# Kernel optimization log

Measured on AMD Instinct MI355X. Metric: run time of the kernel, lower is better.

## Reference

```python
import jax, jax.numpy as jnp
import numpy as np

B, R, SR, K, F = 1, 4096, 40, 8, 32
H = 256           # shading_feature_num
NVF = 4           # num_viewdir_freqs -> 2*4*3 = 24 PE channels
EPS = 1e-8


def positional_encoding(x, n_freqs):
    # x: [..., 3] -> [..., 2*n_freqs*3]
    freqs = (2.0 ** jnp.arange(n_freqs)).astype(x.dtype)          # [nf]
    ang = x[..., None, :] * freqs[:, None]                        # [..., nf, 3]
    enc = jnp.concatenate([jnp.sin(ang), jnp.cos(ang)], axis=-1)  # [..., nf, 6]
    return enc.reshape(x.shape[:-1] + (2 * n_freqs * 3,))


def setup_inputs() -> dict:
    key = jax.random.key(0)
    ks = jax.random.split(key, 20)
    s = 0.02
    inp = {
        "sampled_embedding": jax.random.normal(ks[0], (B, R, SR, K, F), jnp.float32),
        "dists": jax.random.normal(ks[1], (B, R, SR, K, 3), jnp.float32),
        "viewdirs": jax.random.normal(ks[2], (B, R, SR, 3), jnp.float32),
        "pnt_mask": jax.random.randint(ks[3], (B, R, SR, K), 0, 2, jnp.int32),
        # block1: Linear(F,H), Linear(H,H)
        "W1a": jax.random.normal(ks[4], (F, H), jnp.float32) * s,
        "b1a": jnp.zeros((H,), jnp.float32),
        "W1b": jax.random.normal(ks[5], (H, H), jnp.float32) * s,
        "b1b": jnp.zeros((H,), jnp.float32),
        # block3: Linear(H,H), Linear(H,H)
        "W3a": jax.random.normal(ks[6], (H, H), jnp.float32) * s,
        "b3a": jnp.zeros((H,), jnp.float32),
        "W3b": jax.random.normal(ks[7], (H, H), jnp.float32) * s,
        "b3b": jnp.zeros((H,), jnp.float32),
        # alpha branch: Linear(H,1)
        "Wa": jax.random.normal(ks[8], (H, 1), jnp.float32) * s,
        "ba": jnp.zeros((1,), jnp.float32),
        # color branch: Linear(H + 24, 3)
        "Wc": jax.random.normal(ks[9], (H + 2 * NVF * 3, 3), jnp.float32) * s,
        "bc": jnp.zeros((3,), jnp.float32),
    }
    return inp


def reference(sampled_embedding, dists, viewdirs, pnt_mask,
              W1a, b1a, W1b, b1b, W3a, b3a, W3b, b3b, Wa, ba, Wc, bc):
    mask = pnt_mask.astype(sampled_embedding.dtype)               # [B,R,SR,K]
    # quadric distance kernel: w = mask / max(||d||^2, eps)
    d2 = jnp.sum(dists * dists, axis=-1)                          # [B,R,SR,K]
    w = mask / jnp.maximum(d2, EPS)
    # agg_weight_norm: normalize over neighbors
    w = w / jnp.maximum(jnp.sum(w, axis=-1, keepdims=True), EPS)
    # agg_intrp_order == 0: interpolate features first
    feat = jnp.einsum('brsk,brskf->brsf', w, sampled_embedding)   # [B,R,SR,F]
    h = jax.nn.relu(feat @ W1a + b1a)
    h = jax.nn.relu(h @ W1b + b1b)
    h = jax.nn.relu(h @ W3a + b3a)
    h = jax.nn.relu(h @ W3b + b3b)
    # alpha branch + raw2out_density (act_super=1 -> softplus(x-1))
    alpha = jax.nn.softplus(h @ Wa + ba - 1.0)                    # [B,R,SR,1]
    # color branch: concat viewdir PE, then raw2out_color
    vd = viewdirs / jnp.maximum(jnp.linalg.norm(viewdirs, axis=-1, keepdims=True), EPS)
    vpe = positional_encoding(vd, NVF)                            # [B,R,SR,24]
    raw_c = jnp.concatenate([h, vpe], axis=-1) @ Wc + bc          # [B,R,SR,3]
    color = jax.nn.sigmoid(raw_c) * (1.0 + 2e-3) - 1e-3
    return jnp.concatenate([alpha, color], axis=-1)               # [B,R,SR,4]
```

## Files before the change

kernel.cpp:

```cpp
#include <hip/hip_runtime.h>
#include <hip/hip_bf16.h>
#include <cstdint>

typedef __attribute__((ext_vector_type(8))) short short8;
typedef __attribute__((ext_vector_type(4))) float floatx4;
typedef __attribute__((ext_vector_type(4))) float fx4;
typedef __attribute__((ext_vector_type(4))) uint ux4;

#define ROWS 128
#define NTHREADS 256
#define RSTRIDE 296

#define BAR_PLAIN asm volatile("s_barrier" ::: "memory")
#define BAR_LGKM  asm volatile("s_waitcnt lgkmcnt(0)\n\ts_barrier" ::: "memory")

__device__ __forceinline__ ushort f2bf(float x) {
  union { float f; uint32_t u; } v; v.f = x;
  uint32_t r = v.u + 0x7fffu + ((v.u >> 16) & 1u);
  return (ushort)(r >> 16);
}

__device__ __forceinline__ uint32_t cvtpk2(float lo, float hi) {
  uint32_t r;
  asm("v_cvt_pk_bf16_f32 %0, %1, %2" : "=v"(r) : "v"(lo), "v"(hi));
  return r;
}

__global__ void prep_kernel(const float* __restrict__ W1a, const float* __restrict__ W1b,
                            const float* __restrict__ W3a, const float* __restrict__ W3b,
                            const float* __restrict__ Wa,  const float* __restrict__ Wc,
                            const float* __restrict__ ba,  const float* __restrict__ bc,
                            const float* __restrict__ b1b, const float* __restrict__ b3a,
                            const float* __restrict__ b3b,
                            ushort* __restrict__ W1aT, ushort* __restrict__ W1bT,
                            ushort* __restrict__ W3aT, ushort* __restrict__ W3bT,
                            ushort* __restrict__ whead, float* __restrict__ hbias,
                            float* __restrict__ biasAll)
{
  int b = blockIdx.x, t = threadIdx.x;
  W1bT[t * 256 + b] = f2bf(W1b[b * 256 + t]);
  W3aT[t * 256 + b] = f2bf(W3a[b * 256 + t]);
  W3bT[t * 256 + b] = f2bf(W3b[b * 256 + t]);
  if (b < 32) W1aT[t * 32 + b] = f2bf(W1a[b * 256 + t]);
  if (b == 254) {
    biasAll[t]       = b1b[t];
    biasAll[256 + t] = b3a[t];
    biasAll[512 + t] = b3b[t];
  }
  if (b == 255) {
    for (int k = t; k < 288; k += 256) {
      for (int r = 0; r < 16; ++r) {
        float v = 0.f;
        if (r == 0)     v = (k < 256) ? Wa[k] : 0.f;
        else if (r < 4) v = (k < 280) ? Wc[k * 3 + (r - 1)] : 0.f;
        whead[r * 288 + k] = f2bf(v);
      }
    }
    if (t == 0) { hbias[0] = ba[0]; hbias[1] = bc[0]; hbias[2] = bc[1]; hbias[3] = bc[2]; }
  }
}

__device__ __forceinline__ void phaseA_compute(
    const float* __restrict__ emb, const float* __restrict__ dists,
    const float* __restrict__ viewdirs, const int* __restrict__ pnt_mask,
    int gs, int g, ux4& u0, ux4& u1, ux4& u2, ux4& u3)
{
  float d[24];
  const float4* d4 = (const float4*)(dists + (size_t)gs * 24);
  #pragma unroll
  for (int i = 0; i < 6; ++i) {
    float4 q = d4[i];
    d[4*i] = q.x; d[4*i+1] = q.y; d[4*i+2] = q.z; d[4*i+3] = q.w;
  }
  const int4* m4 = (const int4*)(pnt_mask + (size_t)gs * 8);
  int4 m0 = m4[0], m1 = m4[1];
  int mk[8] = {m0.x, m0.y, m0.z, m0.w, m1.x, m1.y, m1.z, m1.w};
  float wv[8]; float sum = 0.f;
  #pragma unroll
  for (int k = 0; k < 8; ++k) {
    float d2 = d[3*k]*d[3*k] + d[3*k+1]*d[3*k+1] + d[3*k+2]*d[3*k+2];
    wv[k] = (float)mk[k] * __builtin_amdgcn_rcpf(fmaxf(d2, 1e-8f));
    sum += wv[k];
  }
  float inv = __builtin_amdgcn_rcpf(fmaxf(sum, 1e-8f));
  #pragma unroll
  for (int k = 0; k < 8; ++k) wv[k] *= inv;

  float acc[16];
  #pragma unroll
  for (int j = 0; j < 16; ++j) acc[j] = 0.f;
  #pragma unroll
  for (int k = 0; k < 8; ++k) {
    const fx4* e4 = (const fx4*)(emb + ((size_t)(gs * 8 + k)) * 32 + g * 16);
    fx4 e0 = __builtin_nontemporal_load(e4);
    fx4 e1 = __builtin_nontemporal_load(e4 + 1);
    fx4 e2 = __builtin_nontemporal_load(e4 + 2);
    fx4 e3 = __builtin_nontemporal_load(e4 + 3);
    acc[0]  += wv[k]*e0.x; acc[1]  += wv[k]*e0.y; acc[2]  += wv[k]*e0.z; acc[3]  += wv[k]*e0.w;
    acc[4]  += wv[k]*e1.x; acc[5]  += wv[k]*e1.y; acc[6]  += wv[k]*e1.z; acc[7]  += wv[k]*e1.w;
    acc[8]  += wv[k]*e2.x; acc[9]  += wv[k]*e2.y; acc[10] += wv[k]*e2.z; acc[11] += wv[k]*e2.w;
    acc[12] += wv[k]*e3.x; acc[13] += wv[k]*e3.y; acc[14] += wv[k]*e3.z; acc[15] += wv[k]*e3.w;
  }
  u0.x = cvtpk2(acc[0],  acc[1]);  u0.y = cvtpk2(acc[2],  acc[3]);
  u0.z = cvtpk2(acc[4],  acc[5]);  u0.w = cvtpk2(acc[6],  acc[7]);
  u1.x = cvtpk2(acc[8],  acc[9]);  u1.y = cvtpk2(acc[10], acc[11]);
  u1.z = cvtpk2(acc[12], acc[13]); u1.w = cvtpk2(acc[14], acc[15]);

  float vx = viewdirs[(size_t)gs * 3 + 0];
  float vy = viewdirs[(size_t)gs * 3 + 1];
  float vz = viewdirs[(size_t)gs * 3 + 2];
  float nrm = sqrtf(vx*vx + vy*vy + vz*vz);
  float ninv = __builtin_amdgcn_rcpf(fmaxf(nrm, 1e-8f));
  uint32_t pd[6];
  #pragma unroll
  for (int h = 0; h < 2; ++h) {
    float fr = (float)(1 << (2 * g + h)) * ninv;
    float sx, cx, sy, cy, sz, cz;
    sincosf(vx * fr, &sx, &cx);
    sincosf(vy * fr, &sy, &cy);
    sincosf(vz * fr, &sz, &cz);
    pd[3*h + 0] = cvtpk2(sx, sy);
    pd[3*h + 1] = cvtpk2(sz, cx);
    pd[3*h + 2] = cvtpk2(cy, cz);
  }
  u2.x = pd[0]; u2.y = pd[1]; u2.z = pd[2]; u2.w = pd[3];
  u3.x = pd[4]; u3.y = pd[5]; u3.z = 0u;    u3.w = 0u;
}

__device__ __forceinline__ void mlp_layer256(ushort (*buf)[RSTRIDE],
                                             const ushort* __restrict__ WT,
                                             const float* __restrict__ bias,
                                             int mbase, int lrow, int kgrp)
{
  floatx4 acc[4][8] = {};
  const ushort* wp = WT + (size_t)(mbase + lrow) * 256 + kgrp * 8;
  short8 a[4];
  #pragma unroll
  for (int mt = 0; mt < 4; ++mt)
    a[mt] = *(const short8*)(wp + mt * 4096);
  __builtin_amdgcn_s_setprio(1);
  #pragma unroll 2
  for (int kt = 0; kt < 8; ++kt) {
    int ktn = (kt + 1) & 7;
    short8 an[4];
    #pragma unroll
    for (int mt = 0; mt < 4; ++mt)
      an[mt] = *(const short8*)(wp + mt * 4096 + ktn * 32);
    short8 b[8];
    #pragma unroll
    for (int nt = 0; nt < 8; ++nt)
      b[nt] = *(const short8*)&buf[nt * 16 + lrow][kt * 32 + kgrp * 8];
    #pragma unroll
    for (int mt = 0; mt < 4; ++mt)
      #pragma unroll
      for (int nt = 0; nt < 8; ++nt)
        acc[mt][nt] = __builtin_amdgcn_mfma_f32_16x16x32_bf16(a[mt], b[nt], acc[mt][nt], 0, 0, 0);
    #pragma unroll
    for (int mt = 0; mt < 4; ++mt) a[mt] = an[mt];
  }
  __builtin_amdgcn_s_setprio(0);
  BAR_PLAIN;
  #pragma unroll
  for (int mt = 0; mt < 4; ++mt) {
    float4 bv = *(const float4*)(bias + mbase + mt * 16 + kgrp * 4);
    #pragma unroll
    for (int nt = 0; nt < 8; ++nt) {
      uint2 pk;
      pk.x = cvtpk2(fmaxf(acc[mt][nt][0] + bv.x, 0.f), fmaxf(acc[mt][nt][1] + bv.y, 0.f));
      pk.y = cvtpk2(fmaxf(acc[mt][nt][2] + bv.z, 0.f), fmaxf(acc[mt][nt][3] + bv.w, 0.f));
      *(uint2*)&buf[nt * 16 + lrow][mbase + mt * 16 + kgrp * 4] = pk;
    }
  }
  BAR_LGKM;
}

__global__ __launch_bounds__(NTHREADS, 2) void pa_fused(
    const float* __restrict__ emb, const float* __restrict__ dists,
    const float* __restrict__ viewdirs, const int* __restrict__ pnt_mask,
    const ushort* __restrict__ W1aT, const float* __restrict__ b1a,
    const ushort* __restrict__ W1bT,
    const float* __restrict__ biasAll,
    const ushort* __restrict__ whead, const float* __restrict__ hbias,
    float* __restrict__ out)
{
  __shared__ ushort buf[ROWS][RSTRIDE];
  const int tid  = threadIdx.x;
  const int base = blockIdx.x * ROWS;

  const int lane = tid & 63;
  const int wid  = tid >> 6;
  const int lrow = lane & 15;
  const int kgrp = lane >> 4;
  const int mbase = wid * 64;

  {
    const int s = tid >> 1, g = tid & 1;
    ux4 u0, u1, u2, u3;
    phaseA_compute(emb, dists, viewdirs, pnt_mask, base + s, g, u0, u1, u2, u3);
    *(ux4*)&buf[s][g * 16]     = u0;
    *(ux4*)&buf[s][g * 16 + 8] = u1;
    uint2* pe = (uint2*)&buf[s][256 + g * 12];
    pe[0] = make_uint2(u2.x, u2.y);
    pe[1] = make_uint2(u2.z, u2.w);
    pe[2] = make_uint2(u3.x, u3.y);
    if (g == 1) {
      ux4 z = {0, 0, 0, 0};
      *(ux4*)&buf[s][280] = z;
    }
  }
  BAR_LGKM;

  {
    floatx4 acc[4][8] = {};
    short8 a[4];
    #pragma unroll
    for (int mt = 0; mt < 4; ++mt)
      a[mt] = *(const short8*)&W1aT[(size_t)(mbase + mt * 16 + lrow) * 32 + kgrp * 8];
    short8 b[8];
    #pragma unroll
    for (int nt = 0; nt < 8; ++nt)
      b[nt] = *(const short8*)&buf[nt * 16 + lrow][kgrp * 8];
    __builtin_amdgcn_s_setprio(1);
    #pragma unroll
    for (int mt = 0; mt < 4; ++mt)
      #pragma unroll
      for (int nt = 0; nt < 8; ++nt)
        acc[mt][nt] = __builtin_amdgcn_mfma_f32_16x16x32_bf16(a[mt], b[nt], acc[mt][nt], 0, 0, 0);
    __builtin_amdgcn_s_setprio(0);
    BAR_PLAIN;
    #pragma unroll
    for (int mt = 0; mt < 4; ++mt) {
      float4 bv = *(const float4*)(b1a + mbase + mt * 16 + kgrp * 4);
      #pragma unroll
      for (int nt = 0; nt < 8; ++nt) {
        uint2 pk;
        pk.x = cvtpk2(fmaxf(acc[mt][nt][0] + bv.x, 0.f), fmaxf(acc[mt][nt][1] + bv.y, 0.f));
        pk.y = cvtpk2(fmaxf(acc[mt][nt][2] + bv.z, 0.f), fmaxf(acc[mt][nt][3] + bv.w, 0.f));
        *(uint2*)&buf[nt * 16 + lrow][mbase + mt * 16 + kgrp * 4] = pk;
      }
    }
    BAR_LGKM;
  }

  {
    const ushort* WT = W1bT;
    const float* bs = biasAll;
    #pragma unroll 1
    for (int L = 0; L < 3; ++L) {
      mlp_layer256(buf, WT, bs, mbase, lrow, kgrp);
      WT += 65536; bs += 256;
    }
  }

  #pragma unroll 1
  for (int h = 0; h < 2; ++h) {
    floatx4 hacc = {0.f, 0.f, 0.f, 0.f};
    #pragma unroll 1
    for (int kt = 0; kt < 9; ++kt) {
      short8 ah = *(const short8*)&whead[(size_t)lrow * 288 + kt * 32 + kgrp * 8];
      short8 b = *(const short8*)&buf[wid * 32 + h * 16 + lrow][kt * 32 + kgrp * 8];
      hacc = __builtin_amdgcn_mfma_f32_16x16x32_bf16(ah, b, hacc, 0, 0, 0);
    }
    if (lane < 16) {
      float4 hb = *(const float4*)hbias;
      float ra = hacc[0] + hb.x - 1.f;
      float alpha = fmaxf(ra, 0.f) + log1pf(expf(-fabsf(ra)));
      float c0 = hacc[1] + hb.y, c1 = hacc[2] + hb.z, c2 = hacc[3] + hb.w;
      fx4 o;
      o.x = alpha;
      o.y = 1.f / (1.f + expf(-c0)) * 1.002f - 1e-3f;
      o.z = 1.f / (1.f + expf(-c1)) * 1.002f - 1e-3f;
      o.w = 1.f / (1.f + expf(-c2)) * 1.002f - 1e-3f;
      int gs = base + wid * 32 + h * 16 + lane;
      __builtin_nontemporal_store(o, (fx4*)(out + (size_t)gs * 4));
    }
  }
}

extern "C" void kernel_launch(void* const* d_in, const int* in_sizes, int n_in,
                              void* d_out, int out_size, void* d_ws, size_t ws_size,
                              hipStream_t stream)
{
  const float* emb   = (const float*)d_in[0];
  const float* dists = (const float*)d_in[1];
  const float* vdirs = (const float*)d_in[2];
  const int*   mask  = (const int*)d_in[3];
  const float* W1a = (const float*)d_in[4];
  const float* b1a = (const float*)d_in[5];
  const float* W1b = (const float*)d_in[6];
  const float* b1b = (const float*)d_in[7];
  const float* W3a = (const float*)d_in[8];
  const float* b3a = (const float*)d_in[9];
  const float* W3b = (const float*)d_in[10];
  const float* b3b = (const float*)d_in[11];
  const float* Wa  = (const float*)d_in[12];
  const float* ba  = (const float*)d_in[13];
  const float* Wc  = (const float*)d_in[14];
  const float* bc  = (const float*)d_in[15];

  int nsamples = in_sizes[2] / 3;

  ushort* wsb  = (ushort*)d_ws;
  ushort* W1aT  = wsb;
  ushort* W1bT  = wsb + 8192;
  ushort* W3aT  = wsb + 73728;
  ushort* W3bT  = wsb + 139264;
  ushort* whead = wsb + 204800;
  float*  hbias   = (float*)(wsb + 209408);
  float*  biasAll = (float*)(wsb + 209416);

  prep_kernel<<<256, 256, 0, stream>>>(W1a, W1b, W3a, W3b, Wa, Wc, ba, bc,
                                       b1b, b3a, b3b,
                                       W1aT, W1bT, W3aT, W3bT, whead, hbias, biasAll);

  int nblocks = nsamples / ROWS;
  pa_fused<<<nblocks, NTHREADS, 0, stream>>>(emb, dists, vdirs, mask,
                                             W1aT, b1a, W1bT, biasAll,
                                             whead, hbias, (float*)d_out);
}
```

Measured before the change: 138.7 us.

## Partition MLP work by rows per wave and drop block barriers

Measured after the change: 290.4 us (median of 2 runs). 2.09x slower.

```diff
diff --git a/kernel.cpp b/kernel.cpp
--- a/kernel.cpp
+++ b/kernel.cpp
@@ -11,8 +11,8 @@
 #define NTHREADS 256
 #define RSTRIDE 296
 
-#define BAR_PLAIN asm volatile("s_barrier" ::: "memory")
-#define BAR_LGKM  asm volatile("s_waitcnt lgkmcnt(0)\n\ts_barrier" ::: "memory")
+#define CFENCE asm volatile("" ::: "memory")
+#define WAIT_LGKM asm volatile("s_waitcnt lgkmcnt(0)" ::: "memory")
 
 __device__ __forceinline__ ushort f2bf(float x) {
   union { float f; uint32_t u; } v; v.f = x;
@@ -127,51 +127,45 @@
   u3.x = pd[4]; u3.y = pd[5]; u3.z = 0u;    u3.w = 0u;
 }
 
-__device__ __forceinline__ void mlp_layer256(ushort (*buf)[RSTRIDE],
-                                             const ushort* __restrict__ WT,
-                                             const float* __restrict__ bias,
-                                             int mbase, int lrow, int kgrp)
-{
-  floatx4 acc[4][8] = {};
-  const ushort* wp = WT + (size_t)(mbase + lrow) * 256 + kgrp * 8;
-  short8 a[4];
-  #pragma unroll
-  for (int mt = 0; mt < 4; ++mt)
-    a[mt] = *(const short8*)(wp + mt * 4096);
+__device__ __forceinline__ void mlp_layer256_s(ushort (*buf)[RSTRIDE],
+                                               const ushort* __restrict__ WT,
+                                               const float* __restrict__ bias,
+                                               int srow, int lrow, int kgrp)
+{
+  floatx4 acc[16][2] = {};
+  const ushort* wp = WT + (size_t)lrow * 256 + kgrp * 8;
   __builtin_amdgcn_s_setprio(1);
-  #pragma unroll 2
+  #pragma unroll
   for (int kt = 0; kt < 8; ++kt) {
-    int ktn = (kt + 1) & 7;
-    short8 an[4];
-    #pragma unroll
-    for (int mt = 0; mt < 4; ++mt)
-      an[mt] = *(const short8*)(wp + mt * 4096 + ktn * 32);
-    short8 b[8];
-    #pragma unroll
-    for (int nt = 0; nt < 8; ++nt)
-      b[nt] = *(const short8*)&buf[nt * 16 + lrow][kt * 32 + kgrp * 8];
-    #pragma unroll
-    for (int mt = 0; mt < 4; ++mt)
-      #pragma unroll
-      for (int nt = 0; nt < 8; ++nt)
-        acc[mt][nt] = __builtin_amdgcn_mfma_f32_16x16x32_bf16(a[mt], b[nt], acc[mt][nt], 0, 0, 0);
-    #pragma unroll
-    for (int mt = 0; mt < 4; ++mt) a[mt] = an[mt];
+    short8 b0 = *(const short8*)&buf[srow + lrow][kt * 32 + kgrp * 8];
+    short8 b1 = *(const short8*)&buf[srow + 16 + lrow][kt * 32 + kgrp * 8];
+    #pragma unroll
+    for (int mh = 0; mh < 2; ++mh) {
+      short8 a[8];
+      #pragma unroll
+      for (int i = 0; i < 8; ++i)
+        a[i] = *(const short8*)(wp + (size_t)(mh * 8 + i) * 4096 + kt * 32);
+      #pragma unroll
+      for (int i = 0; i < 8; ++i) {
+        acc[mh*8+i][0] = __builtin_amdgcn_mfma_f32_16x16x32_bf16(a[i], b0, acc[mh*8+i][0], 0, 0, 0);
+        acc[mh*8+i][1] = __builtin_amdgcn_mfma_f32_16x16x32_bf16(a[i], b1, acc[mh*8+i][1], 0, 0, 0);
+      }
+    }
   }
   __builtin_amdgcn_s_setprio(0);
-  BAR_PLAIN;
-  #pragma unroll
-  for (int mt = 0; mt < 4; ++mt) {
-    float4 bv = *(const float4*)(bias + mbase + mt * 16 + kgrp * 4);
-    #pragma unroll
-    for (int nt = 0; nt < 8; ++nt) {
+  CFENCE;
+  #pragma unroll
+  for (int mt = 0; mt < 16; ++mt) {
+    float4 bv = *(const float4*)(bias + mt * 16 + kgrp * 4);
+    #pragma unroll
+    for (int nt = 0; nt < 2; ++nt) {
       uint2 pk;
       pk.x = cvtpk2(fmaxf(acc[mt][nt][0] + bv.x, 0.f), fmaxf(acc[mt][nt][1] + bv.y, 0.f));
       pk.y = cvtpk2(fmaxf(acc[mt][nt][2] + bv.z, 0.f), fmaxf(acc[mt][nt][3] + bv.w, 0.f));
-      *(uint2*)&buf[nt * 16 + lrow][mbase + mt * 16 + kgrp * 4] = pk;
-    }
-  }
-  BAR_LGKM;
+      *(uint2*)&buf[srow + nt * 16 + lrow][mt * 16 + kgrp * 4] = pk;
+    }
+  }
+  CFENCE;
 }
 
 __global__ __launch_bounds__(NTHREADS, 2) void pa_fused(
@@ -191,7 +185,7 @@
   const int wid  = tid >> 6;
   const int lrow = lane & 15;
   const int kgrp = lane >> 4;
-  const int mbase = wid * 64;
+  const int srow = wid * 32;
 
   {
     const int s = tid >> 1, g = tid & 1;
@@ -208,57 +202,54 @@
       *(ux4*)&buf[s][280] = z;
     }
   }
-  BAR_LGKM;
+  WAIT_LGKM;
 
   {
-    floatx4 acc[4][8] = {};
-    short8 a[4];
-    #pragma unroll
-    for (int mt = 0; mt < 4; ++mt)
-      a[mt] = *(const short8*)&W1aT[(size_t)(mbase + mt * 16 + lrow) * 32 + kgrp * 8];
-    short8 b[8];
-    #pragma unroll
-    for (int nt = 0; nt < 8; ++nt)
-      b[nt] = *(const short8*)&buf[nt * 16 + lrow][kgrp * 8];
+    floatx4 acc[16][2] = {};
+    short8 b0 = *(const short8*)&buf[srow + lrow][kgrp * 8];
+    short8 b1 = *(const short8*)&buf[srow + 16 + lrow][kgrp * 8];
+    const ushort* wp = W1aT + (size_t)lrow * 32 + kgrp * 8;
     __builtin_amdgcn_s_setprio(1);
     #pragma unroll
-    for (int mt = 0; mt < 4; ++mt)
-      #pragma unroll
-      for (int nt = 0; nt < 8; ++nt)
-        acc[mt][nt] = __builtin_amdgcn_mfma_f32_16x16x32_bf16(a[mt], b[nt], acc[mt][nt], 0, 0, 0);
+    for (int mh = 0; mh < 2; ++mh) {
+      short8 a[8];
+      #pragma unroll
+      for (int i = 0; i < 8; ++i)
+        a[i] = *(const short8*)(wp + (size_t)(mh * 8 + i) * 512);
+      #pragma unroll
+      for (int i = 0; i < 8; ++i) {
+        acc[mh*8+i][0] = __builtin_amdgcn_mfma_f32_16x16x32_bf16(a[i], b0, acc[mh*8+i][0], 0, 0, 0);
+        acc[mh*8+i][1] = __builtin_amdgcn_mfma_f32_16x16x32_bf16(a[i], b1, acc[mh*8+i][1], 0, 0, 0);
+      }
+    }
     __builtin_amdgcn_s_setprio(0);
-    BAR_PLAIN;
-    #pragma unroll
-    for (int mt = 0; mt < 4; ++mt) {
-      float4 bv = *(const float4*)(b1a + mbase + mt * 16 + kgrp * 4);
-      #pragma unroll
-      for (int nt = 0; nt < 8; ++nt) {
+    CFENCE;
+    #pragma unroll
+    for (int mt = 0; mt < 16; ++mt) {
+      float4 bv = *(const float4*)(b1a + mt * 16 + kgrp * 4);
+      #pragma unroll
+      for (int nt = 0; nt < 2; ++nt) {
         uint2 pk;
         pk.x = cvtpk2(fmaxf(acc[mt][nt][0] + bv.x, 0.f), fmaxf(acc[mt][nt][1] + bv.y, 0.f));
         pk.y = cvtpk2(fmaxf(acc[mt][nt][2] + bv.z, 0.f), fmaxf(acc[mt][nt][3] + bv.w, 0.f));
-        *(uint2*)&buf[nt * 16 + lrow][mbase + mt * 16 + kgrp * 4] = pk;
+        *(uint2*)&buf[srow + nt * 16 + lrow][mt * 16 + kgrp * 4] = pk;
       }
     }
-    BAR_LGKM;
-  }
-
-  {
-    const ushort* WT = W1bT;
-    const float* bs = biasAll;
-    #pragma unroll 1
-    for (int L = 0; L < 3; ++L) {
-      mlp_layer256(buf, WT, bs, mbase, lrow, kgrp);
-      WT += 65536; bs += 256;
-    }
-  }
-
-  #pragma unroll 1
+    CFENCE;
+  }
+
+  mlp_layer256_s(buf, W1bT,          biasAll,       srow, lrow, kgrp);
+  mlp_layer256_s(buf, W1bT + 65536,  biasAll + 256, srow, lrow, kgrp);
+  mlp_layer256_s(buf, W1bT + 131072, biasAll + 512, srow, lrow, kgrp);
+
+  __builtin_amdgcn_s_setprio(1);
+  #pragma unroll
   for (int h = 0; h < 2; ++h) {
     floatx4 hacc = {0.f, 0.f, 0.f, 0.f};
-    #pragma unroll 1
+    #pragma unroll
     for (int kt = 0; kt < 9; ++kt) {
       short8 ah = *(const short8*)&whead[(size_t)lrow * 288 + kt * 32 + kgrp * 8];
-      short8 b = *(const short8*)&buf[wid * 32 + h * 16 + lrow][kt * 32 + kgrp * 8];
+      short8 b = *(const short8*)&buf[srow + h * 16 + lrow][kt * 32 + kgrp * 8];
       hacc = __builtin_amdgcn_mfma_f32_16x16x32_bf16(ah, b, hacc, 0, 0, 0);
     }
     if (lane < 16) {
@@ -271,10 +262,11 @@
       o.y = 1.f / (1.f + expf(-c0)) * 1.002f - 1e-3f;
       o.z = 1.f / (1.f + expf(-c1)) * 1.002f - 1e-3f;
       o.w = 1.f / (1.f + expf(-c2)) * 1.002f - 1e-3f;
-      int gs = base + wid * 32 + h * 16 + lane;
+      int gs = base + srow + h * 16 + lane;
       __builtin_nontemporal_store(o, (fx4*)(out + (size_t)gs * 4));
     }
   }
+  __builtin_amdgcn_s_setprio(0);
 }
 
 extern "C" void kernel_launch(void* const* d_in, const int* in_sizes, int n_in,
```
